# Kernel optimization log

Hardware: AMD Instinct MI355X
Metric: run time of the kernel (lower is better)

## Reference

```python
import jax, jax.numpy as jnp
import numpy as np

E, H, F, T, K = 32, 1024, 512, 1024, 8

def setup_inputs() -> dict:
    key = jax.random.key(0)
    k1, k2, k3, k4, k5 = jax.random.split(key, 5)
    return {
        "hidden_states": jax.random.normal(k1, (T, H), dtype=jnp.float32),
        "top_k_index": jax.random.randint(k2, (T, K), 0, E),
        "top_k_weights": jax.random.uniform(k3, (T, K), dtype=jnp.float32),
        "gate_up_proj": jax.random.normal(k4, (E, 2 * F, H), dtype=jnp.float32),
        "down_proj": jax.random.normal(k5, (E, H, F), dtype=jnp.float32),
    }

def reference(hidden_states, top_k_index, top_k_weights, gate_up_proj, down_proj):
    n_experts = gate_up_proj.shape[0]
    T_ = hidden_states.shape[0]
    # Combine routing weights into dense [T, E] map (duplicates accumulate,
    # matching torch's index_add_ semantics).
    w = jnp.zeros((T_, n_experts), dtype=hidden_states.dtype)
    w = w.at[jnp.arange(T_)[:, None], top_k_index].add(top_k_weights)
    ffn = down_proj.shape[-1]

    def step(final, params):
        Wgu, Wd, we = params  # [2F,H], [H,F], [T]
        gu = hidden_states @ Wgu.T            # [T, 2F]
        gate, up = gu[:, :ffn], gu[:, ffn:]
        out = (jax.nn.silu(gate) * up) @ Wd.T  # [T, H]
        return final + we[:, None] * out, None

    final, _ = jax.lax.scan(step, jnp.zeros_like(hidden_states),
                            (gate_up_proj, down_proj, w.T))
    return final
```

## Files before the change

kernel.cpp:

```cpp
#include <hip/hip_runtime.h>
#include <hip/hip_bf16.h>

#define NE     32
#define HD     1024
#define FF     512
#define NT     1024
#define TOPK   8
#define NPAIR  (NT * TOPK)
#define MAXT2  96

typedef __attribute__((ext_vector_type(8))) short  bf16x8;
typedef __attribute__((ext_vector_type(4))) float  f32x4;

__device__ __forceinline__ unsigned short f2bf_rne(float f) {
    unsigned u = __float_as_uint(f);
    u += 0x7FFFu + ((u >> 16) & 1u);
    return (unsigned short)(u >> 16);
}
__device__ __forceinline__ unsigned pk2(float x, float y) {
    __hip_bfloat162 h = __float22bfloat162_rn(float2{x, y});
    union { __hip_bfloat162 h; unsigned u; } c;
    c.h = h;
    return c.u;
}
__device__ __forceinline__ uint4 pk8v(float4 a, float4 b) {
    uint4 r;
    r.x = pk2(a.x, a.y); r.y = pk2(a.z, a.w);
    r.z = pk2(b.x, b.y); r.w = pk2(b.z, b.w);
    return r;
}
__device__ __forceinline__ void gload16(const void* g, void* l) {
    __builtin_amdgcn_global_load_lds(
        (const __attribute__((address_space(1))) unsigned int*)g,
        (__attribute__((address_space(3))) unsigned int*)l, 16, 0, 0);
}
__device__ __forceinline__ bf16x8 pkfrag(const void* p0, const void* p1) {
    f32x4 a = *(const f32x4*)p0;
    f32x4 b = *(const f32x4*)p1;
    union { unsigned u[4]; bf16x8 v; } r;
    r.u[0] = pk2(a[0], a[1]); r.u[1] = pk2(a[2], a[3]);
    r.u[2] = pk2(b[0], b[1]); r.u[3] = pk2(b[2], b[3]);
    return r.v;
}
#define MFMA16(a, b, c) __builtin_amdgcn_mfma_f32_16x16x32_bf16(a, b, c, 0, 0, 0)

#define OFF_XG (128u * 1024u)
#define OFF_AB (OFF_XG + 8320u * 2048u)
#define OFF_O  (OFF_AB + 8320u * 1024u)

__global__ __launch_bounds__(1024) void k_route(const int* __restrict__ idx,
                                                const float* __restrict__ tkw,
                                                int* __restrict__ meta) {
    __shared__ int sc[NE], scur[NE], soff[NE + 1];
    __shared__ int ste[MAXT2], stm[MAXT2], snt;
    int tid = threadIdx.x;
    if (tid < NE) { sc[tid] = 0; scur[tid] = 0; }
    __syncthreads();
    int e8[TOPK];
#pragma unroll
    for (int j = 0; j < TOPK; j++) { e8[j] = idx[tid * TOPK + j]; atomicAdd(&sc[e8[j]], 1); }
    __syncthreads();
    if (tid == 0) {
        int off = 0, nt = 0;
        for (int e = 0; e < NE; e++) {
            soff[e] = off;
            for (int s = 0; s < sc[e]; s += 128) { ste[nt] = e; stm[nt] = s; nt++; }
            off += sc[e];
        }
        soff[NE] = off; snt = nt;
    }
    __syncthreads();
    int*   tok_list = meta + 256;
    float* w_list   = (float*)(meta + 8448);
    int*   posmap   = meta + 16640;
#pragma unroll
    for (int j = 0; j < TOPK; j++) {
        int e = e8[j];
        int p = soff[e] + atomicAdd(&scur[e], 1);
        tok_list[p] = tid;
        w_list[p]   = tkw[tid * TOPK + j];
        posmap[tid * TOPK + j] = p;
    }
    if (tid <= NE) meta[1 + tid] = soff[tid];
    if (tid == 0)  meta[0] = snt;
    if (tid < MAXT2) { meta[64 + tid] = (tid < snt) ? ste[tid] : 0;
                       meta[160 + tid] = (tid < snt) ? stm[tid] : 0; }
}

__global__ void k_gather(const float* __restrict__ hs, const int* __restrict__ meta,
                         unsigned short* __restrict__ Xg) {
    int i = blockIdx.x * blockDim.x + threadIdx.x;
    int p = i >> 7, c = (i & 127) << 3;
    int tok = meta[256 + p];
    float4 a = *(const float4*)(hs + (size_t)tok * HD + c);
    float4 b = *(const float4*)(hs + (size_t)tok * HD + c + 4);
    *(uint4*)(Xg + (size_t)p * HD + c) = pk8v(a, b);
}

__global__ __launch_bounds__(256) void k_mm1(
        const unsigned short* __restrict__ Xg, const float* __restrict__ wgu,
        const int* __restrict__ meta, unsigned short* __restrict__ A) {
    int lid = blockIdx.y * MAXT2 + blockIdx.x;
    int wsw = (lid & 7) * 192 + (lid >> 3);
    int bx = wsw % MAXT2, by = wsw / MAXT2;
    int numt = meta[0];
    if (bx >= numt) return;
    int e   = meta[64 + bx], m0 = meta[160 + bx];
    int seg = meta[1 + e];
    int nrows = meta[2 + e] - seg - m0;
    if (nrows > 128) nrows = 128;
    int c0 = by * 32;

    __shared__ __align__(16) unsigned char Xs[2][8192];
    __shared__ __align__(16) unsigned char Ws[2][8192];
    __shared__ float wrows[128];
    int tid = threadIdx.x;
    const float* w_list = (const float*)(meta + 8448);
    if (tid < 128) wrows[tid] = (tid < nrows) ? w_list[seg + m0 + tid] : 0.f;

    int wave = tid >> 6, lane = tid & 63, lr = lane & 15, lk = lane >> 4;

    const unsigned char* xsrc[2];
    const unsigned char* wsrc[2];
    unsigned ldsoff[2];
#pragma unroll
    for (int i = 0; i < 2; i++) {
        unsigned Lp = (unsigned)(wave * 2 + i) * 1024u + (unsigned)lane * 16u;
        ldsoff[i] = Lp;
        unsigned xr = Lp >> 6, xc = (Lp & 63u) ^ (((Lp >> 7) & 3u) << 4);
        xsrc[i] = (const unsigned char*)Xg + (size_t)(seg + m0 + xr) * (HD * 2) + xc;
        unsigned wr_ = Lp >> 7, wc = (Lp & 127u) ^ ((wr_ & 7u) << 4);
        unsigned grow = (wr_ < 32) ? (c0 + wr_) : (FF + c0 + (wr_ - 32));
        wsrc[i] = (const unsigned char*)wgu + ((size_t)e * (2 * FF) + grow) * (HD * 4) + wc;
    }
    unsigned aoff[2];
#pragma unroll
    for (int mf = 0; mf < 2; mf++) {
        unsigned row = wave * 32 + mf * 16 + lr;
        aoff[mf] = row * 64 + (((unsigned)lk * 16) ^ (((row >> 1) & 3u) << 4));
    }
    unsigned boff0[4], boff1[4];
#pragma unroll
    for (int nf = 0; nf < 4; nf++) {
        unsigned row = nf * 16 + lr;
        unsigned swz = (row & 7u) << 4;
        boff0[nf] = row * 128 + (((unsigned)lk * 32) ^ swz);
        boff1[nf] = row * 128 + (((unsigned)lk * 32 + 16) ^ swz);
    }

    f32x4 accg[2][2] = {}, accu[2][2] = {};
#pragma unroll
    for (int i = 0; i < 2; i++) {
        gload16(xsrc[i], &Xs[0][ldsoff[i]]);
        gload16(wsrc[i], &Ws[0][ldsoff[i]]);
    }
    __syncthreads();

    int cur = 0;
    for (int t = 0; t < HD / 32; ++t) {
        if (t + 1 < HD / 32) {
#pragma unroll
            for (int i = 0; i < 2; i++) {
                xsrc[i] += 64; wsrc[i] += 128;
                gload16(xsrc[i], &Xs[cur ^ 1][ldsoff[i]]);
                gload16(wsrc[i], &Ws[cur ^ 1][ldsoff[i]]);
            }
        }
        const unsigned char* xb = Xs[cur];
        const unsigned char* wb = Ws[cur];
        bf16x8 af0 = *(const bf16x8*)(xb + aoff[0]);
        bf16x8 af1 = *(const bf16x8*)(xb + aoff[1]);
#pragma unroll
        for (int j = 0; j < 2; j++) {
            bf16x8 bg = pkfrag(wb + boff0[j],     wb + boff1[j]);
            bf16x8 bu = pkfrag(wb + boff0[j + 2], wb + boff1[j + 2]);
            accg[0][j] = MFMA16(af0, bg, accg[0][j]);
            accg[1][j] = MFMA16(af1, bg, accg[1][j]);
            accu[0][j] = MFMA16(af0, bu, accu[0][j]);
            accu[1][j] = MFMA16(af1, bu, accu[1][j]);
        }
        __syncthreads();
        cur ^= 1;
    }
#pragma unroll
    for (int mf = 0; mf < 2; mf++)
#pragma unroll
        for (int q = 0; q < 4; q++) {
            int r = wave * 32 + mf * 16 + lk * 4 + q;
            if (r < nrows) {
                float w = wrows[r];
#pragma unroll
                for (int j = 0; j < 2; j++) {
                    float g = accg[mf][j][q], u = accu[mf][j][q];
                    float act = (g / (1.f + __expf(-g))) * u * w;
                    A[(size_t)(seg + m0 + r) * FF + c0 + j * 16 + lr] = f2bf_rne(act);
                }
            }
        }
}

__global__ __launch_bounds__(256) void k_mm2(
        const unsigned short* __restrict__ A, const float* __restrict__ wd,
        const int* __restrict__ meta, float* __restrict__ O) {
    int lid = blockIdx.y * MAXT2 + blockIdx.x;
    int wsw = (lid & 7) * 192 + (lid >> 3);
    int bx = wsw % MAXT2, by = wsw / MAXT2;
    int numt = meta[0];
    if (bx >= numt) return;
    int e   = meta[64 + bx], m0 = meta[160 + bx];
    int seg = meta[1 + e];
    int nrows = meta[2 + e] - seg - m0;
    if (nrows > 128) nrows = 128;
    int n0 = by * 64;

    __shared__ __align__(16) unsigned char Xs[2][8192];
    __shared__ __align__(16) unsigned char Ws[2][8192];
    int tid = threadIdx.x;
    int wave = tid >> 6, lane = tid & 63, lr = lane & 15, lk = lane >> 4;

    const unsigned char* xsrc[2];
    const unsigned char* wsrc[2];
    unsigned ldsoff[2];
#pragma unroll
    for (int i = 0; i < 2; i++) {
        unsigned Lp = (unsigned)(wave * 2 + i) * 1024u + (unsigned)lane * 16u;
        ldsoff[i] = Lp;
        unsigned xr = Lp >> 6, xc = (Lp & 63u) ^ (((Lp >> 7) & 3u) << 4);
        xsrc[i] = (const unsigned char*)A + (size_t)(seg + m0 + xr) * (FF * 2) + xc;
        unsigned wr_ = Lp >> 7, wc = (Lp & 127u) ^ ((wr_ & 7u) << 4);
        wsrc[i] = (const unsigned char*)wd + ((size_t)e * HD + n0 + wr_) * (FF * 4) + wc;
    }
    unsigned aoff[2];
#pragma unroll
    for (int mf = 0; mf < 2; mf++) {
        unsigned row = wave * 32 + mf * 16 + lr;
        aoff[mf] = row * 64 + (((unsigned)lk * 16) ^ (((row >> 1) & 3u) << 4));
    }
    unsigned boff0[4], boff1[4];
#pragma unroll
    for (int nf = 0; nf < 4; nf++) {
        unsigned row = nf * 16 + lr;
        unsigned swz = (row & 7u) << 4;
        boff0[nf] = row * 128 + (((unsigned)lk * 32) ^ swz);
        boff1[nf] = row * 128 + (((unsigned)lk * 32 + 16) ^ swz);
    }

    f32x4 acc[2][4] = {};
#pragma unroll
    for (int i = 0; i < 2; i++) {
        gload16(xsrc[i], &Xs[0][ldsoff[i]]);
        gload16(wsrc[i], &Ws[0][ldsoff[i]]);
    }
    __syncthreads();

    int cur = 0;
    for (int t = 0; t < FF / 32; ++t) {
        if (t + 1 < FF / 32) {
#pragma unroll
            for (int i = 0; i < 2; i++) {
                xsrc[i] += 64; wsrc[i] += 128;
                gload16(xsrc[i], &Xs[cur ^ 1][ldsoff[i]]);
                gload16(wsrc[i], &Ws[cur ^ 1][ldsoff[i]]);
            }
        }
        const unsigned char* xb = Xs[cur];
        const unsigned char* wb = Ws[cur];
        bf16x8 af0 = *(const bf16x8*)(xb + aoff[0]);
        bf16x8 af1 = *(const bf16x8*)(xb + aoff[1]);
#pragma unroll
        for (int nf = 0; nf < 4; nf++) {
            bf16x8 b = pkfrag(wb + boff0[nf], wb + boff1[nf]);
            acc[0][nf] = MFMA16(af0, b, acc[0][nf]);
            acc[1][nf] = MFMA16(af1, b, acc[1][nf]);
        }
        __syncthreads();
        cur ^= 1;
    }
#pragma unroll
    for (int mf = 0; mf < 2; mf++)
#pragma unroll
        for (int q = 0; q < 4; q++) {
            int r = wave * 32 + mf * 16 + lk * 4 + q;
            if (r < nrows) {
#pragma unroll
                for (int nf = 0; nf < 4; nf++)
                    O[(size_t)(seg + m0 + r) * HD + n0 + nf * 16 + lr] = acc[mf][nf][q];
            }
        }
}

__global__ void k_reduce(const float* __restrict__ O, const int* __restrict__ posmap,
                         float* __restrict__ out) {
    int i = blockIdx.x * blockDim.x + threadIdx.x;
    int t = i >> 8, c4 = i & 255;
    float4 acc = make_float4(0.f, 0.f, 0.f, 0.f);
#pragma unroll
    for (int k = 0; k < TOPK; k++) {
        int p = posmap[t * TOPK + k];
        float4 v = ((const float4*)(O + (size_t)p * HD))[c4];
        acc.x += v.x; acc.y += v.y; acc.z += v.z; acc.w += v.w;
    }
    ((float4*)out)[i] = acc;
}

extern "C" void kernel_launch(void* const* d_in, const int* in_sizes, int n_in,
                              void* d_out, int out_size, void* d_ws, size_t ws_size,
                              hipStream_t stream) {
    const float* hs  = (const float*)d_in[0];
    const int*   idx = (const int*)  d_in[1];
    const float* tkw = (const float*)d_in[2];
    const float* wgu = (const float*)d_in[3];
    const float* wd  = (const float*)d_in[4];
    float* out = (float*)d_out;

    char* ws = (char*)d_ws;
    int* meta = (int*)ws;
    unsigned short* Xg   = (unsigned short*)(ws + OFF_XG);
    unsigned short* A_bf = (unsigned short*)(ws + OFF_AB);
    float* O_rows        = (float*)(ws + OFF_O);
    const int* posmap    = meta + 16640;

    k_route<<<1, 1024, 0, stream>>>(idx, tkw, meta);
    k_gather<<<NPAIR * (HD / 8) / 256, 256, 0, stream>>>(hs, meta, Xg);
    dim3 g1(MAXT2, FF / 32);
    k_mm1<<<g1, 256, 0, stream>>>(Xg, wgu, meta, A_bf);
    dim3 g2(MAXT2, HD / 64);
    k_mm2<<<g2, 256, 0, stream>>>(A_bf, wd, meta, O_rows);
    k_reduce<<<NT * HD / 4 / 256, 256, 0, stream>>>(O_rows, posmap, out);
}
```

Before: 156.5 us.

## Triple-buffer LDS in expert GEMMs with a single barrier per k-step

Both grouped GEMM kernels move from double to triple LDS buffering and prefetch two k-steps ahead. Explicit s_waitcnt vmcnt waits plus one s_barrier per iteration replace the two __syncthreads, so more global-to-LDS traffic stays in flight while MFMAs run. The launch grid becomes 1-D with a different block-to-tile mapping, and the per-row routing weights are read straight from global memory instead of being staged in shared memory. LDS use per block grows, which may lower occupancy, and the hand-written waitcnt depends on the exact number of loads issued per stage.

```diff
diff --git a/kernel.cpp b/kernel.cpp
--- a/kernel.cpp
+++ b/kernel.cpp
@@ -23,7 +23,7 @@
     c.h = h;
     return c.u;
 }
-__device__ __forceinline__ uint4 pk8v(float4 a, float4 b) {
+__device__ __forceinline__ uint4 pk8q(float4 a, float4 b) {
     uint4 r;
     r.x = pk2(a.x, a.y); r.y = pk2(a.z, a.w);
     r.z = pk2(b.x, b.y); r.w = pk2(b.z, b.w);
@@ -94,15 +94,16 @@
     int tok = meta[256 + p];
     float4 a = *(const float4*)(hs + (size_t)tok * HD + c);
     float4 b = *(const float4*)(hs + (size_t)tok * HD + c + 4);
-    *(uint4*)(Xg + (size_t)p * HD + c) = pk8v(a, b);
+    *(uint4*)(Xg + (size_t)p * HD + c) = pk8q(a, b);
 }
 
 __global__ __launch_bounds__(256) void k_mm1(
         const unsigned short* __restrict__ Xg, const float* __restrict__ wgu,
-        const int* __restrict__ meta, unsigned short* __restrict__ A) {
-    int lid = blockIdx.y * MAXT2 + blockIdx.x;
+        const int* __restrict__ meta, const float* __restrict__ w_list,
+        unsigned short* __restrict__ A) {
+    int lid = blockIdx.x;
     int wsw = (lid & 7) * 192 + (lid >> 3);
-    int bx = wsw % MAXT2, by = wsw / MAXT2;
+    int bx = wsw >> 4, by = wsw & 15;
     int numt = meta[0];
     if (bx >= numt) return;
     int e   = meta[64 + bx], m0 = meta[160 + bx];
@@ -111,13 +112,9 @@
     if (nrows > 128) nrows = 128;
     int c0 = by * 32;
 
-    __shared__ __align__(16) unsigned char Xs[2][8192];
-    __shared__ __align__(16) unsigned char Ws[2][8192];
-    __shared__ float wrows[128];
+    __shared__ __align__(16) unsigned char Xs[3][8192];
+    __shared__ __align__(16) unsigned char Ws[3][8192];
     int tid = threadIdx.x;
-    const float* w_list = (const float*)(meta + 8448);
-    if (tid < 128) wrows[tid] = (tid < nrows) ? w_list[seg + m0 + tid] : 0.f;
-
     int wave = tid >> 6, lane = tid & 63, lr = lane & 15, lk = lane >> 4;
 
     const unsigned char* xsrc[2];
@@ -150,24 +147,30 @@
 
     f32x4 accg[2][2] = {}, accu[2][2] = {};
 #pragma unroll
+    for (int i = 0; i < 2; i++) { gload16(xsrc[i], &Xs[0][ldsoff[i]]); gload16(wsrc[i], &Ws[0][ldsoff[i]]); }
+#pragma unroll
     for (int i = 0; i < 2; i++) {
-        gload16(xsrc[i], &Xs[0][ldsoff[i]]);
-        gload16(wsrc[i], &Ws[0][ldsoff[i]]);
-    }
-    __syncthreads();
-
-    int cur = 0;
-    for (int t = 0; t < HD / 32; ++t) {
-        if (t + 1 < HD / 32) {
+        xsrc[i] += 64; wsrc[i] += 128;
+        gload16(xsrc[i], &Xs[1][ldsoff[i]]); gload16(wsrc[i], &Ws[1][ldsoff[i]]);
+    }
+
+    const int NSTEP = HD / 32;
+    for (int t = 0; t < NSTEP; ++t) {
+        if (t + 1 < NSTEP) asm volatile("s_waitcnt vmcnt(4)" ::: "memory");
+        else               asm volatile("s_waitcnt vmcnt(0)" ::: "memory");
+        __builtin_amdgcn_s_barrier();
+        __builtin_amdgcn_sched_barrier(0);
+        if (t + 2 < NSTEP) {
+            int nb = (t + 2) % 3;
 #pragma unroll
             for (int i = 0; i < 2; i++) {
                 xsrc[i] += 64; wsrc[i] += 128;
-                gload16(xsrc[i], &Xs[cur ^ 1][ldsoff[i]]);
-                gload16(wsrc[i], &Ws[cur ^ 1][ldsoff[i]]);
+                gload16(xsrc[i], &Xs[nb][ldsoff[i]]);
+                gload16(wsrc[i], &Ws[nb][ldsoff[i]]);
             }
         }
-        const unsigned char* xb = Xs[cur];
-        const unsigned char* wb = Ws[cur];
+        const unsigned char* xb = Xs[t % 3];
+        const unsigned char* wb = Ws[t % 3];
         bf16x8 af0 = *(const bf16x8*)(xb + aoff[0]);
         bf16x8 af1 = *(const bf16x8*)(xb + aoff[1]);
 #pragma unroll
@@ -179,8 +182,6 @@
             accu[0][j] = MFMA16(af0, bu, accu[0][j]);
             accu[1][j] = MFMA16(af1, bu, accu[1][j]);
         }
-        __syncthreads();
-        cur ^= 1;
     }
 #pragma unroll
     for (int mf = 0; mf < 2; mf++)
@@ -188,7 +189,7 @@
         for (int q = 0; q < 4; q++) {
             int r = wave * 32 + mf * 16 + lk * 4 + q;
             if (r < nrows) {
-                float w = wrows[r];
+                float w = w_list[seg + m0 + r];
 #pragma unroll
                 for (int j = 0; j < 2; j++) {
                     float g = accg[mf][j][q], u = accu[mf][j][q];
@@ -202,9 +203,9 @@
 __global__ __launch_bounds__(256) void k_mm2(
         const unsigned short* __restrict__ A, const float* __restrict__ wd,
         const int* __restrict__ meta, float* __restrict__ O) {
-    int lid = blockIdx.y * MAXT2 + blockIdx.x;
+    int lid = blockIdx.x;
     int wsw = (lid & 7) * 192 + (lid >> 3);
-    int bx = wsw % MAXT2, by = wsw / MAXT2;
+    int bx = wsw >> 4, by = wsw & 15;
     int numt = meta[0];
     if (bx >= numt) return;
     int e   = meta[64 + bx], m0 = meta[160 + bx];
@@ -213,8 +214,8 @@
     if (nrows > 128) nrows = 128;
     int n0 = by * 64;
 
-    __shared__ __align__(16) unsigned char Xs[2][8192];
-    __shared__ __align__(16) unsigned char Ws[2][8192];
+    __shared__ __align__(16) unsigned char Xs[3][8192];
+    __shared__ __align__(16) unsigned char Ws[3][8192];
     int tid = threadIdx.x;
     int wave = tid >> 6, lane = tid & 63, lr = lane & 15, lk = lane >> 4;
 
@@ -247,24 +248,30 @@
 
     f32x4 acc[2][4] = {};
 #pragma unroll
+    for (int i = 0; i < 2; i++) { gload16(xsrc[i], &Xs[0][ldsoff[i]]); gload16(wsrc[i], &Ws[0][ldsoff[i]]); }
+#pragma unroll
     for (int i = 0; i < 2; i++) {
-        gload16(xsrc[i], &Xs[0][ldsoff[i]]);
-        gload16(wsrc[i], &Ws[0][ldsoff[i]]);
-    }
-    __syncthreads();
-
-    int cur = 0;
-    for (int t = 0; t < FF / 32; ++t) {
-        if (t + 1 < FF / 32) {
+        xsrc[i] += 64; wsrc[i] += 128;
+        gload16(xsrc[i], &Xs[1][ldsoff[i]]); gload16(wsrc[i], &Ws[1][ldsoff[i]]);
+    }
+
+    const int NSTEP = FF / 32;
+    for (int t = 0; t < NSTEP; ++t) {
+        if (t + 1 < NSTEP) asm volatile("s_waitcnt vmcnt(4)" ::: "memory");
+        else               asm volatile("s_waitcnt vmcnt(0)" ::: "memory");
+        __builtin_amdgcn_s_barrier();
+        __builtin_amdgcn_sched_barrier(0);
+        if (t + 2 < NSTEP) {
+            int nb = (t + 2) % 3;
 #pragma unroll
             for (int i = 0; i < 2; i++) {
                 xsrc[i] += 64; wsrc[i] += 128;
-                gload16(xsrc[i], &Xs[cur ^ 1][ldsoff[i]]);
-                gload16(wsrc[i], &Ws[cur ^ 1][ldsoff[i]]);
+                gload16(xsrc[i], &Xs[nb][ldsoff[i]]);
+                gload16(wsrc[i], &Ws[nb][ldsoff[i]]);
             }
         }
-        const unsigned char* xb = Xs[cur];
-        const unsigned char* wb = Ws[cur];
+        const unsigned char* xb = Xs[t % 3];
+        const unsigned char* wb = Ws[t % 3];
         bf16x8 af0 = *(const bf16x8*)(xb + aoff[0]);
         bf16x8 af1 = *(const bf16x8*)(xb + aoff[1]);
 #pragma unroll
@@ -273,8 +280,6 @@
             acc[0][nf] = MFMA16(af0, b, acc[0][nf]);
             acc[1][nf] = MFMA16(af1, b, acc[1][nf]);
         }
-        __syncthreads();
-        cur ^= 1;
     }
 #pragma unroll
     for (int mf = 0; mf < 2; mf++)
@@ -318,13 +323,12 @@
     unsigned short* Xg   = (unsigned short*)(ws + OFF_XG);
     unsigned short* A_bf = (unsigned short*)(ws + OFF_AB);
     float* O_rows        = (float*)(ws + OFF_O);
+    const float* w_list  = (const float*)(meta + 8448);
     const int* posmap    = meta + 16640;
 
     k_route<<<1, 1024, 0, stream>>>(idx, tkw, meta);
     k_gather<<<NPAIR * (HD / 8) / 256, 256, 0, stream>>>(hs, meta, Xg);
-    dim3 g1(MAXT2, FF / 32);
-    k_mm1<<<g1, 256, 0, stream>>>(Xg, wgu, meta, A_bf);
-    dim3 g2(MAXT2, HD / 64);
-    k_mm2<<<g2, 256, 0, stream>>>(A_bf, wd, meta, O_rows);
+    k_mm1<<<MAXT2 * 16, 256, 0, stream>>>(Xg, wgu, meta, w_list, A_bf);
+    k_mm2<<<MAXT2 * 16, 256, 0, stream>>>(A_bf, wd, meta, O_rows);
     k_reduce<<<NT * HD / 4 / 256, 256, 0, stream>>>(O_rows, posmap, out);
 }
```

Result: no change. 156.8 us (+0.2%).
